# Performance work log

Measured on AMD Instinct MI355X. Metric: run time of the kernel, lower is better.

The kernel has to match this reference:

```python
import jax, jax.numpy as jnp
import numpy as np

B, C, N = 4, 256, 512
CQ = C // 4
SIGMA = 15.0
PICK = 0  # args.picked_point_num
FACTOR = 180.0 / (np.pi * SIGMA)
BN_EPS = 1e-5


def _angle_embed(angles, W, b):
    """SinusoidalPositionalEmbedding (interleaved sin/cos, detached) + Linear proj."""
    d = W.shape[0]
    div_term = jnp.exp(jnp.arange(0, d, 2, dtype=jnp.float32) * (-np.log(10000.0) / d))
    omegas = (angles * FACTOR)[..., None] * div_term  # (..., d/2)
    # torch cat([sin, cos], dim=2) on (-1, d/2, 1) then view -> interleaved [s0,c0,s1,c1,...]
    emb = jnp.stack([jnp.sin(omegas), jnp.cos(omegas)], axis=-1).reshape(*angles.shape, d)
    emb = jax.lax.stop_gradient(emb)  # .detach() in torch
    return emb @ W.T + b


def setup_inputs() -> dict:
    key = jax.random.key(0)
    ks = jax.random.split(key, 16)
    s = 0.05
    return {
        "x": jax.random.normal(ks[0], (B, C, N), jnp.float32),
        "pca": jax.random.normal(ks[1], (B, C, N), jnp.float32),
        "angle_lrf": jax.random.uniform(ks[2], (B, N, N), jnp.float32, 0.0, np.pi),
        "angle_pca": jax.random.uniform(ks[3], (B, N), jnp.float32, 0.0, np.pi),
        "Wkp": jax.random.normal(ks[4], (CQ, C), jnp.float32) * s,
        "Wk": jax.random.normal(ks[5], (CQ, C), jnp.float32) * s,
        "Wv": jax.random.normal(ks[6], (C, C), jnp.float32) * s,
        "Wvp": jax.random.normal(ks[7], (C, C), jnp.float32) * s,
        "emb1_W": jax.random.normal(ks[8], (CQ, CQ), jnp.float32) * s,
        "emb1_b": jnp.zeros((CQ,), jnp.float32),
        "emb2_W": jax.random.normal(ks[9], (CQ, CQ), jnp.float32) * s,
        "emb2_b": jnp.zeros((CQ,), jnp.float32),
        "lin_W": jax.random.normal(ks[10], (C, C), jnp.float32) * s,
        "lin_b": jnp.zeros((C,), jnp.float32),
        "bn_gamma": jnp.ones((C,), jnp.float32),
        "bn_beta": jnp.zeros((C,), jnp.float32),
    }


def reference(x, pca, angle_lrf, angle_pca, Wkp, Wk, Wv, Wvp,
              emb1_W, emb1_b, emb2_W, emb2_b, lin_W, lin_b, bn_gamma, bn_beta):
    # q uses the k_conv_pca weight (weight tying in __init__)
    x_q = jnp.einsum('oc,bcn->bno', Wkp, x)            # (B,N,CQ)
    k_lrf = jnp.einsum('oc,bcn->bon', Wk, x)           # (B,CQ,N)
    k_pca = jnp.einsum('oc,bcn->bon', Wkp, pca)        # (B,CQ,N)
    energy_lrf = jnp.einsum('bno,bom->bnm', x_q, k_lrf)
    energy_pca = jnp.einsum('bno,bom->bnm', x_q, k_pca)
    e1 = _angle_embed(angle_lrf, emb1_W, emb1_b)       # (B,N,N,CQ) relative-angle bias
    energy_lrf = energy_lrf + jnp.einsum('bnc,bnmc->bnm', x_q, e1)
    e2 = _angle_embed(angle_pca, emb2_W, emb2_b)       # (B,N,CQ)
    energy_pca = energy_pca + jnp.einsum('bnc,bmc->bnm', x_q, e2)
    energy = jax.nn.softmax(energy_lrf + energy_pca, axis=-1)
    # extra column renormalization
    energy = energy / (1e-12 + energy.sum(axis=1, keepdims=True))
    point_relation = energy[:, PICK:PICK + 1, :]       # (B,1,N)
    v_lrf = jnp.einsum('oc,bcn->bon', Wv, x)
    v_pca = jnp.einsum('oc,bcn->bon', Wvp, pca)
    x_lrf = jnp.einsum('bon,bnm->bom', v_lrf, energy)
    x_pca = jnp.einsum('bon,bnm->bom', v_pca, energy)
    x_r = 0.5 * x_lrf + 0.5 * x_pca
    z = jnp.einsum('oc,bcn->bon', lin_W, x - x_r) + lin_b[None, :, None]
    # BatchNorm1d (training-mode batch stats, biased var)
    mu = z.mean(axis=(0, 2), keepdims=True)
    var = z.var(axis=(0, 2), keepdims=True)
    y = bn_gamma[None, :, None] * (z - mu) * jax.lax.rsqrt(var + BN_EPS) + bn_beta[None, :, None]
    out = x + jax.nn.gelu(y, approximate=False)
    return out, point_relation
```

## Files before the change

### kernel.cpp

```cpp
#include <hip/hip_runtime.h>
#include <math.h>

#define FCT 3.81971863420548805845f
#define DIVK 0.28782313662425575f

using bf16x8 = __attribute__((ext_vector_type(8))) short;
using f32x4  = __attribute__((ext_vector_type(4))) float;

__device__ inline short f2bf(float f) {
    union { float f; unsigned u; } v; v.f = f;
    unsigned r = v.u + 0x7FFFu + ((v.u >> 16) & 1u);
    return (short)(r >> 16);
}
__device__ inline float bf2f(short s) {
    union { unsigned u; float f; } v;
    v.u = ((unsigned)(unsigned short)s) << 16;
    return v.f;
}
__device__ inline unsigned pk2(float lo, float hi) {
    return ((unsigned)(unsigned short)f2bf(hi) << 16) | (unsigned)(unsigned short)f2bf(lo);
}

__global__ __launch_bounds__(256) void k_prep(
    const float* __restrict__ Wkp, const float* __restrict__ Wk,
    const float* __restrict__ Wv, const float* __restrict__ Wvp,
    const float* __restrict__ linW, const float* __restrict__ e1W,
    const float* __restrict__ x, const float* __restrict__ pca,
    short* __restrict__ Wcatb, short* __restrict__ InTb)
{
    __shared__ float ts[64][65];
    const int bid = blockIdx.x;
    if (bid < 704) {
        const int r = bid;
        for (int k = threadIdx.x; k < 512; k += 256) {
            float v = 0.f;
            if (r < 64) { if (k < 256) v = Wkp[r*256 + k]; }
            else if (r < 128) { int o = r-64;  v = (k<256) ? Wk[o*256+k]  : Wkp[o*256 + k-256]; }
            else if (r < 384) { int o = r-128; v = (k<256) ? Wv[o*256+k]  : Wvp[o*256 + k-256]; }
            else if (r < 640) { int o = r-384; if (k<256) v = linW[o*256+k]; }
            else {
                int o = r-640;
                if (k < 256) {
                    float a = 0.f;
                    for (int j = 0; j < 64; ++j) a = fmaf(e1W[j*64 + o], Wkp[j*256 + k], a);
                    v = a;
                }
            }
            Wcatb[(size_t)r*512 + k] = f2bf(v);
        }
    } else {
        const int id = bid - 704;
        const int b  = id >> 6;
        const int kt = (id >> 3) & 7;
        const int nt = id & 7;
        const int k0 = kt*64, n0 = nt*64;
        const float* src = (k0 < 256) ? (x + ((size_t)b*256 + k0)*512)
                                      : (pca + ((size_t)b*256 + (k0-256))*512);
        #pragma unroll
        for (int i = 0; i < 16; ++i) {
            int idx = threadIdx.x + 256*i;
            int r = idx >> 6, c = idx & 63;
            ts[r][c] = src[(size_t)r*512 + n0 + c];
        }
        __syncthreads();
        short* dst = InTb + (size_t)b*512*512;
        #pragma unroll
        for (int i = 0; i < 16; ++i) {
            int idx = threadIdx.x + 256*i;
            int n = idx >> 6, k = idx & 63;
            dst[(size_t)(n0+n)*512 + k0 + k] = f2bf(ts[k][n]);
        }
    }
}

__global__ __launch_bounds__(256) void k_gemm1(
    const short* __restrict__ Wcatb, const short* __restrict__ InTb,
    short* __restrict__ xqb, float* __restrict__ Ktf, short* __restrict__ vsumb,
    float* __restrict__ linx, float* __restrict__ q1T)
{
    const int bid = blockIdx.x;
    const int b  = bid / 176;
    const int rt = (bid / 16) % 11;
    const int ct = bid % 16;
    const int r0 = rt*64, c0 = ct*32;
    const int w = threadIdx.x >> 6, lane = threadIdx.x & 63;
    const int lr = lane & 15, lg = lane >> 4;

    const short* ap  = Wcatb + (size_t)(r0 + w*16 + lr)*512 + 8*lg;
    const short* bp0 = InTb + (size_t)b*512*512 + (size_t)(c0 + lr)*512 + 8*lg;
    const short* bp1 = bp0 + 16*512;

    f32x4 acc0 = {0.f,0.f,0.f,0.f}, acc1 = {0.f,0.f,0.f,0.f};
    #pragma unroll 4
    for (int kk = 0; kk < 512; kk += 32) {
        bf16x8 a  = *(const bf16x8*)(ap  + kk);
        bf16x8 b0 = *(const bf16x8*)(bp0 + kk);
        bf16x8 b1 = *(const bf16x8*)(bp1 + kk);
        acc0 = __builtin_amdgcn_mfma_f32_16x16x32_bf16(a, b0, acc0, 0, 0, 0);
        acc1 = __builtin_amdgcn_mfma_f32_16x16x32_bf16(a, b1, acc1, 0, 0, 0);
    }
    const int rowb = r0 + w*16 + lg*4;
    const int col0 = c0 + lr;
    if (r0 == 0) {
        #pragma unroll
        for (int j = 0; j < 4; ++j) {
            xqb[((size_t)b*512 + col0)*64 + rowb + j]      = f2bf(acc0[j]);
            xqb[((size_t)b*512 + col0 + 16)*64 + rowb + j] = f2bf(acc1[j]);
        }
    } else if (r0 == 64) {
        #pragma unroll
        for (int j = 0; j < 4; ++j) {
            Ktf[((size_t)b*64 + rowb-64 + j)*512 + col0]      = acc0[j];
            Ktf[((size_t)b*64 + rowb-64 + j)*512 + col0 + 16] = acc1[j];
        }
    } else if (r0 < 384) {
        #pragma unroll
        for (int j = 0; j < 4; ++j) {
            vsumb[((size_t)b*256 + rowb-128 + j)*512 + col0]      = f2bf(acc0[j]);
            vsumb[((size_t)b*256 + rowb-128 + j)*512 + col0 + 16] = f2bf(acc1[j]);
        }
    } else if (r0 < 640) {
        #pragma unroll
        for (int j = 0; j < 4; ++j) {
            linx[((size_t)b*256 + rowb-384 + j)*512 + col0]      = acc0[j];
            linx[((size_t)b*256 + rowb-384 + j)*512 + col0 + 16] = acc1[j];
        }
    } else {
        #pragma unroll
        for (int j = 0; j < 4; ++j) {
            q1T[((size_t)b*512 + col0)*64 + rowb-640 + j]      = acc0[j];
            q1T[((size_t)b*512 + col0 + 16)*64 + rowb-640 + j] = acc1[j];
        }
    }
}

__global__ __launch_bounds__(256) void k_e2t(
    const float* __restrict__ angle_pca, const float* __restrict__ e2W,
    const float* __restrict__ Ktf, short* __restrict__ KtT)
{
    const int b  = blockIdx.x >> 3;
    const int m0 = (blockIdx.x & 7) * 64;
    __shared__ float emb_s[64][65];
    __shared__ float e2w_s[64][65];
    const int t = threadIdx.x;
    #pragma unroll
    for (int i = 0; i < 16; ++i) {
        int idx = t + 256*i;
        e2w_s[idx >> 6][idx & 63] = e2W[idx];
    }
    {
        const int m = t >> 2, q = t & 3;
        const float a = angle_pca[b*512 + m0 + m] * FCT;
        #pragma unroll
        for (int i = q*8; i < q*8+8; ++i) {
            float arg = a * __expf(-(float)i * DIVK);
            emb_s[m][2*i]   = __sinf(arg);
            emb_s[m][2*i+1] = __cosf(arg);
        }
    }
    __syncthreads();
    const int o = t & 63, wid = t >> 6;
    for (int mi = wid; mi < 64; mi += 4) {
        float acc = Ktf[((size_t)b*64 + o)*512 + m0 + mi];
        #pragma unroll 8
        for (int k = 0; k < 64; ++k) acc = fmaf(e2w_s[o][k], emb_s[mi][k], acc);
        KtT[((size_t)b*512 + m0 + mi)*64 + o] = f2bf(acc);
    }
}

__global__ __launch_bounds__(256) void k_qk(
    const short* __restrict__ xqb, const short* __restrict__ KtT,
    float* __restrict__ S)
{
    const int bid = blockIdx.x;
    const int b  = bid / 128;
    const int rt = (bid / 16) % 8;
    const int ct = bid % 16;
    const int r0 = rt*64, c0 = ct*32;
    const int w = threadIdx.x >> 6, lane = threadIdx.x & 63;
    const int lr = lane & 15, lg = lane >> 4;
    const short* ap  = xqb + ((size_t)b*512 + r0 + w*16 + lr)*64 + 8*lg;
    const short* bp0 = KtT + ((size_t)b*512 + c0 + lr)*64 + 8*lg;
    const short* bp1 = bp0 + 16*64;
    f32x4 acc0 = {0.f,0.f,0.f,0.f}, acc1 = {0.f,0.f,0.f,0.f};
    #pragma unroll
    for (int kk = 0; kk < 64; kk += 32) {
        bf16x8 a  = *(const bf16x8*)(ap  + kk);
        bf16x8 b0 = *(const bf16x8*)(bp0 + kk);
        bf16x8 b1 = *(const bf16x8*)(bp1 + kk);
        acc0 = __builtin_amdgcn_mfma_f32_16x16x32_bf16(a, b0, acc0, 0, 0, 0);
        acc1 = __builtin_amdgcn_mfma_f32_16x16x32_bf16(a, b1, acc1, 0, 0, 0);
    }
    const int rowb = r0 + w*16 + lg*4;
    const int col0 = c0 + lr;
    float* Sb = S + (size_t)b*512*512;
    #pragma unroll
    for (int j = 0; j < 4; ++j) {
        Sb[(size_t)(rowb+j)*512 + col0]      = acc0[j];
        Sb[(size_t)(rowb+j)*512 + col0 + 16] = acc1[j];
    }
}

__global__ __launch_bounds__(256) void k_energy2(
    const float* __restrict__ S, const float* __restrict__ q1T,
    const float* __restrict__ angle_lrf, short* __restrict__ ETb)
{
    const int b  = blockIdx.x >> 7;
    const int n0 = (blockIdx.x & 127) * 4;
    __shared__ float qs[4][64];
    __shared__ float divs[32];
    __shared__ float4 red[256];
    const int t = threadIdx.x;
    if (t < 64) {
        #pragma unroll
        for (int i = 0; i < 4; ++i) qs[i][t] = q1T[((size_t)b*512 + n0 + i)*64 + t];
    } else if (t < 96) {
        divs[t-64] = __expf(-(float)(t-64) * DIVK);
    }
    __syncthreads();
    float acc[4][2], av[4][2];
    #pragma unroll
    for (int i = 0; i < 4; ++i) {
        const float2 sv = *(const float2*)&S[((size_t)b*512 + n0 + i)*512 + 2*t];
        const float2 an = *(const float2*)&angle_lrf[((size_t)b*512 + n0 + i)*512 + 2*t];
        acc[i][0] = sv.x; acc[i][1] = sv.y;
        av[i][0] = an.x * FCT; av[i][1] = an.y * FCT;
    }
    for (int j = 0; j < 32; ++j) {
        const float d = divs[j];
        const float w0 = qs[0][2*j], w1 = qs[0][2*j+1];
        const float u0 = qs[1][2*j], u1 = qs[1][2*j+1];
        const float v0 = qs[2][2*j], v1 = qs[2][2*j+1];
        const float y0 = qs[3][2*j], y1 = qs[3][2*j+1];
        #pragma unroll
        for (int m = 0; m < 2; ++m) {
            float a0 = av[0][m]*d, a1 = av[1][m]*d, a2 = av[2][m]*d, a3 = av[3][m]*d;
            acc[0][m] = fmaf(w0, __sinf(a0), fmaf(w1, __cosf(a0), acc[0][m]));
            acc[1][m] = fmaf(u0, __sinf(a1), fmaf(u1, __cosf(a1), acc[1][m]));
            acc[2][m] = fmaf(v0, __sinf(a2), fmaf(v1, __cosf(a2), acc[2][m]));
            acc[3][m] = fmaf(y0, __sinf(a3), fmaf(y1, __cosf(a3), acc[3][m]));
        }
    }
    float4 v;
    v.x = fmaxf(acc[0][0], acc[0][1]); v.y = fmaxf(acc[1][0], acc[1][1]);
    v.z = fmaxf(acc[2][0], acc[2][1]); v.w = fmaxf(acc[3][0], acc[3][1]);
    red[t] = v; __syncthreads();
    for (int s = 128; s > 0; s >>= 1) {
        if (t < s) {
            float4 o = red[t+s], m2 = red[t];
            m2.x = fmaxf(m2.x,o.x); m2.y = fmaxf(m2.y,o.y);
            m2.z = fmaxf(m2.z,o.z); m2.w = fmaxf(m2.w,o.w);
            red[t] = m2;
        }
        __syncthreads();
    }
    const float4 mx = red[0]; __syncthreads();
    float p[4][2];
    p[0][0] = __expf(acc[0][0]-mx.x); p[0][1] = __expf(acc[0][1]-mx.x);
    p[1][0] = __expf(acc[1][0]-mx.y); p[1][1] = __expf(acc[1][1]-mx.y);
    p[2][0] = __expf(acc[2][0]-mx.z); p[2][1] = __expf(acc[2][1]-mx.z);
    p[3][0] = __expf(acc[3][0]-mx.w); p[3][1] = __expf(acc[3][1]-mx.w);
    v.x = p[0][0]+p[0][1]; v.y = p[1][0]+p[1][1];
    v.z = p[2][0]+p[2][1]; v.w = p[3][0]+p[3][1];
    red[t] = v; __syncthreads();
    for (int s = 128; s > 0; s >>= 1) {
        if (t < s) {
            float4 o = red[t+s];
            red[t].x += o.x; red[t].y += o.y; red[t].z += o.z; red[t].w += o.w;
        }
        __syncthreads();
    }
    const float4 tot = red[0];
    const float i0 = 1.f/tot.x, i1 = 1.f/tot.y, i2 = 1.f/tot.z, i3 = 1.f/tot.w;
    short* Eb = ETb + (size_t)b*512*512;
    #pragma unroll
    for (int m = 0; m < 2; ++m) {
        uint2 u;
        u.x = pk2(p[0][m]*i0, p[1][m]*i1);
        u.y = pk2(p[2][m]*i2, p[3][m]*i3);
        *(uint2*)(Eb + (size_t)(2*t + m)*512 + n0) = u;
    }
}

__global__ __launch_bounds__(256) void k_colsum(
    const short* __restrict__ ETb, float* __restrict__ rc, float* __restrict__ out)
{
    const int row  = blockIdx.x*4 + (threadIdx.x >> 6);
    const int lane = threadIdx.x & 63;
    const uint4 u4 = *(const uint4*)(ETb + (size_t)row*512 + lane*8);
    float s = 0.f;
    unsigned uu[4] = {u4.x, u4.y, u4.z, u4.w};
    #pragma unroll
    for (int i = 0; i < 4; ++i) {
        union { unsigned u; float f; } lo, hi;
        lo.u = uu[i] << 16; hi.u = uu[i] & 0xFFFF0000u;
        s += lo.f + hi.f;
    }
    #pragma unroll
    for (int off = 32; off > 0; off >>= 1) s += __shfl_xor(s, off, 64);
    if (lane == 0) {
        const float r = 1.f / (1e-12f + s);
        rc[row] = r;
        out[(size_t)4*256*512 + row] = bf2f((short)(u4.x & 0xFFFFu)) * r;
    }
}

__global__ __launch_bounds__(256) void k_xr2(
    const short* __restrict__ vsumb, const short* __restrict__ ETb,
    const float* __restrict__ rc, short* __restrict__ xrT)
{
    const int bid = blockIdx.x;
    const int b  = bid / 64;
    const int rt = (bid / 16) % 4;
    const int ct = bid % 16;
    const int r0 = rt*64, c0 = ct*32;
    const int w = threadIdx.x >> 6, lane = threadIdx.x & 63;
    const int lr = lane & 15, lg = lane >> 4;
    const short* ap  = vsumb + (size_t)b*256*512 + (size_t)(r0 + w*16 + lr)*512 + 8*lg;
    const short* bp0 = ETb + (size_t)b*512*512 + (size_t)(c0 + lr)*512 + 8*lg;
    const short* bp1 = bp0 + 16*512;
    f32x4 acc0 = {0.f,0.f,0.f,0.f}, acc1 = {0.f,0.f,0.f,0.f};
    #pragma unroll 4
    for (int kk = 0; kk < 512; kk += 32) {
        bf16x8 a  = *(const bf16x8*)(ap  + kk);
        bf16x8 b0 = *(const bf16x8*)(bp0 + kk);
        bf16x8 b1 = *(const bf16x8*)(bp1 + kk);
        acc0 = __builtin_amdgcn_mfma_f32_16x16x32_bf16(a, b0, acc0, 0, 0, 0);
        acc1 = __builtin_amdgcn_mfma_f32_16x16x32_bf16(a, b1, acc1, 0, 0, 0);
    }
    const int rowb = r0 + w*16 + lg*4;
    const int m0 = c0 + lr, m1 = m0 + 16;
    const float s0 = 0.5f * rc[b*512 + m0];
    const float s1 = 0.5f * rc[b*512 + m1];
    short* xb = xrT + (size_t)b*512*256;
    uint2 u;
    u.x = pk2(acc0[0]*s0, acc0[1]*s0);
    u.y = pk2(acc0[2]*s0, acc0[3]*s0);
    *(uint2*)(xb + (size_t)m0*256 + rowb) = u;
    u.x = pk2(acc1[0]*s1, acc1[1]*s1);
    u.y = pk2(acc1[2]*s1, acc1[3]*s1);
    *(uint2*)(xb + (size_t)m1*256 + rowb) = u;
}

__global__ __launch_bounds__(256) void k_z2(
    const short* __restrict__ Wcatb, const short* __restrict__ xrT,
    const float* __restrict__ linx, const float* __restrict__ lin_b,
    float* __restrict__ z)
{
    const int bid = blockIdx.x;
    const int b  = bid / 64;
    const int rt = (bid / 16) % 4;
    const int ct = bid % 16;
    const int r0 = rt*64, c0 = ct*32;
    const int w = threadIdx.x >> 6, lane = threadIdx.x & 63;
    const int lr = lane & 15, lg = lane >> 4;
    const short* ap  = Wcatb + (size_t)(384 + r0 + w*16 + lr)*512 + 8*lg;
    const short* bp0 = xrT + (size_t)b*512*256 + (size_t)(c0 + lr)*256 + 8*lg;
    const short* bp1 = bp0 + 16*256;
    f32x4 acc0 = {0.f,0.f,0.f,0.f}, acc1 = {0.f,0.f,0.f,0.f};
    #pragma unroll
    for (int kk = 0; kk < 256; kk += 32) {
        bf16x8 a  = *(const bf16x8*)(ap  + kk);
        bf16x8 b0 = *(const bf16x8*)(bp0 + kk);
        bf16x8 b1 = *(const bf16x8*)(bp1 + kk);
        acc0 = __builtin_amdgcn_mfma_f32_16x16x32_bf16(a, b0, acc0, 0, 0, 0);
        acc1 = __builtin_amdgcn_mfma_f32_16x16x32_bf16(a, b1, acc1, 0, 0, 0);
    }
    const int rowb = r0 + w*16 + lg*4;
    const int col0 = c0 + lr;
    const float* Lb = linx + (size_t)b*256*512;
    float* zb = z + (size_t)b*256*512;
    #pragma unroll
    for (int j = 0; j < 4; ++j) {
        float lb = lin_b[rowb+j];
        zb[(size_t)(rowb+j)*512 + col0]      = Lb[(size_t)(rowb+j)*512 + col0]      - acc0[j] + lb;
        zb[(size_t)(rowb+j)*512 + col0 + 16] = Lb[(size_t)(rowb+j)*512 + col0 + 16] - acc1[j] + lb;
    }
}

__global__ __launch_bounds__(256) void k_stats(
    const float* __restrict__ z, float* __restrict__ stat)
{
    const int c = blockIdx.x;
    const int t = threadIdx.x;
    float s = 0.f, s2 = 0.f;
    for (int i = t; i < 2048; i += 256) {
        int b = i >> 9, n = i & 511;
        float v = z[((size_t)b*256 + c)*512 + n];
        s += v; s2 = fmaf(v, v, s2);
    }
    __shared__ float r1[256], r2[256];
    r1[t] = s; r2[t] = s2;
    __syncthreads();
    for (int st = 128; st > 0; st >>= 1) {
        if (t < st) { r1[t] += r1[t+st]; r2[t] += r2[t+st]; }
        __syncthreads();
    }
    if (t == 0) { stat[c] = r1[0]; stat[256 + c] = r2[0]; }
}

__global__ __launch_bounds__(256) void k_final(
    const float* __restrict__ x, const float* __restrict__ z,
    const float* __restrict__ stat, const float* __restrict__ gamma,
    const float* __restrict__ beta, float* __restrict__ out)
{
    const int gid = blockIdx.x*256 + threadIdx.x;
    const int base = gid * 4;
    const int c = (base >> 9) & 255;
    const float mu  = stat[c] * (1.f/2048.f);
    const float var = stat[256 + c] * (1.f/2048.f) - mu*mu;
    const float gsc = gamma[c] * rsqrtf(var + 1e-5f);
    const float bt  = beta[c];
    const float4 zv = *(const float4*)&z[base];
    const float4 xv = *(const float4*)&x[base];
    float4 ov;
    {
        float y = (zv.x - mu)*gsc + bt;
        ov.x = xv.x + 0.5f*y*(1.f + erff(y*0.70710678118654752f));
        y = (zv.y - mu)*gsc + bt;
        ov.y = xv.y + 0.5f*y*(1.f + erff(y*0.70710678118654752f));
        y = (zv.z - mu)*gsc + bt;
        ov.z = xv.z + 0.5f*y*(1.f + erff(y*0.70710678118654752f));
        y = (zv.w - mu)*gsc + bt;
        ov.w = xv.w + 0.5f*y*(1.f + erff(y*0.70710678118654752f));
    }
    *(float4*)&out[base] = ov;
}

extern "C" void kernel_launch(void* const* d_in, const int* in_sizes, int n_in,
                              void* d_out, int out_size, void* d_ws, size_t ws_size,
                              hipStream_t stream)
{
    const float* x         = (const float*)d_in[0];
    const float* pca       = (const float*)d_in[1];
    const float* angle_lrf = (const float*)d_in[2];
    const float* angle_pca = (const float*)d_in[3];
    const float* Wkp       = (const float*)d_in[4];
    const float* Wk        = (const float*)d_in[5];
    const float* Wv        = (const float*)d_in[6];
    const float* Wvp       = (const float*)d_in[7];
    const float* e1W       = (const float*)d_in[8];
    const float* e2W       = (const float*)d_in[10];
    const float* linW      = (const float*)d_in[12];
    const float* linb      = (const float*)d_in[13];
    const float* gamma     = (const float*)d_in[14];
    const float* beta      = (const float*)d_in[15];

    char* w = (char*)d_ws;
    short* Wcatb = (short*)(w + 0);
    short* InTb  = (short*)(w + 720896);
    short* vsumb = (short*)(w + 2818048);
    short* KtT   = (short*)(w + 3866624);
    short* ETb   = (short*)(w + 4128768);
    float* rc    = (float*)(w + 6225920);
    short* xrT   = (short*)(w + 6234112);
    float* stat  = (float*)(w + 7282688);
    float* S     = (float*)(w + 7284736);
    float* Ktf   = (float*)(w + 7284736);
    float* z     = (float*)(w + 7284736);
    short* xqb   = (short*)(w + 11479040);
    float* q1T   = (float*)(w + 11741184);
    float* linx  = (float*)(w + 12789760);
    float* out   = (float*)d_out;

    k_prep   <<<960, 256, 0, stream>>>(Wkp, Wk, Wv, Wvp, linW, e1W, x, pca, Wcatb, InTb);
    k_gemm1  <<<704, 256, 0, stream>>>(Wcatb, InTb, xqb, Ktf, vsumb, linx, q1T);
    k_e2t    <<<32,  256, 0, stream>>>(angle_pca, e2W, Ktf, KtT);
    k_qk     <<<512, 256, 0, stream>>>(xqb, KtT, S);
    k_energy2<<<512, 256, 0, stream>>>(S, q1T, angle_lrf, ETb);
    k_colsum <<<512, 256, 0, stream>>>(ETb, rc, out);
    k_xr2    <<<256, 256, 0, stream>>>(vsumb, ETb, rc, xrT);
    k_z2     <<<256, 256, 0, stream>>>(Wcatb, xrT, linx, linb, z);
    k_stats  <<<256, 256, 0, stream>>>(z, stat);
    k_final  <<<512, 256, 0, stream>>>(x, z, stat, gamma, beta, out);
}
```

Baseline: 88.00 us.

## Fuse colsum and BN stats into producers, use native revolution sin/cos

Removes the separate column-sum and BatchNorm-statistics kernels. Their work moves into k_energy2 and the z GEMM as atomicAdd accumulations, with buffers zeroed in k_prep. The energy and embedding kernels call hardware v_sin/v_cos on arguments pre-scaled to revolutions, avoiding range reduction. The block max/sum reductions become wave shuffles. The e2 projection is restructured with a transposed weight and register accumulation, and k_prep processes 4 rows per block. Atomics add nondeterministic summation order and contention on colsum, and there is accuracy risk from the raw sin/cos instructions.

```diff
diff --git a/kernel.cpp b/kernel.cpp
--- a/kernel.cpp
+++ b/kernel.cpp
@@ -1,7 +1,7 @@
 #include <hip/hip_runtime.h>
 #include <math.h>
 
-#define FCT 3.81971863420548805845f
+#define FCT_REV 0.6079271018540267f
 #define DIVK 0.28782313662425575f
 
 using bf16x8 = __attribute__((ext_vector_type(8))) short;
@@ -20,36 +20,57 @@
 __device__ inline unsigned pk2(float lo, float hi) {
     return ((unsigned)(unsigned short)f2bf(hi) << 16) | (unsigned)(unsigned short)f2bf(lo);
 }
+__device__ inline float sinrev(float x) {
+    float r; asm("v_sin_f32 %0, %1" : "=v"(r) : "v"(x)); return r;
+}
+__device__ inline float cosrev(float x) {
+    float r; asm("v_cos_f32 %0, %1" : "=v"(r) : "v"(x)); return r;
+}
 
 __global__ __launch_bounds__(256) void k_prep(
     const float* __restrict__ Wkp, const float* __restrict__ Wk,
     const float* __restrict__ Wv, const float* __restrict__ Wvp,
     const float* __restrict__ linW, const float* __restrict__ e1W,
+    const float* __restrict__ e2W,
     const float* __restrict__ x, const float* __restrict__ pca,
-    short* __restrict__ Wcatb, short* __restrict__ InTb)
+    short* __restrict__ Wcatb, short* __restrict__ InTb,
+    float* __restrict__ e2Wt, float* __restrict__ stat, float* __restrict__ colsum)
 {
     __shared__ float ts[64][65];
     const int bid = blockIdx.x;
-    if (bid < 704) {
-        const int r = bid;
-        for (int k = threadIdx.x; k < 512; k += 256) {
-            float v = 0.f;
-            if (r < 64) { if (k < 256) v = Wkp[r*256 + k]; }
-            else if (r < 128) { int o = r-64;  v = (k<256) ? Wk[o*256+k]  : Wkp[o*256 + k-256]; }
-            else if (r < 384) { int o = r-128; v = (k<256) ? Wv[o*256+k]  : Wvp[o*256 + k-256]; }
-            else if (r < 640) { int o = r-384; if (k<256) v = linW[o*256+k]; }
-            else {
-                int o = r-640;
-                if (k < 256) {
-                    float a = 0.f;
-                    for (int j = 0; j < 64; ++j) a = fmaf(e1W[j*64 + o], Wkp[j*256 + k], a);
-                    v = a;
+    const int t = threadIdx.x;
+    if (bid < 176) {
+        if (bid == 0) {
+            for (int i = t; i < 2048; i += 256) colsum[i] = 0.f;
+            for (int i = t; i < 512; i += 256) stat[i] = 0.f;
+        } else if (bid == 1) {
+            for (int i = t; i < 4096; i += 256) {
+                int k = i >> 6, o = i & 63;
+                e2Wt[k*64 + o] = e2W[o*64 + k];
+            }
+        }
+        #pragma unroll
+        for (int rr = 0; rr < 4; ++rr) {
+            const int r = bid*4 + rr;
+            for (int k = t; k < 512; k += 256) {
+                float v = 0.f;
+                if (r < 64) { if (k < 256) v = Wkp[r*256 + k]; }
+                else if (r < 128) { int o = r-64;  v = (k<256) ? Wk[o*256+k]  : Wkp[o*256 + k-256]; }
+                else if (r < 384) { int o = r-128; v = (k<256) ? Wv[o*256+k]  : Wvp[o*256 + k-256]; }
+                else if (r < 640) { int o = r-384; if (k<256) v = linW[o*256+k]; }
+                else {
+                    int o = r-640;
+                    if (k < 256) {
+                        float a = 0.f;
+                        for (int j = 0; j < 64; ++j) a = fmaf(e1W[j*64 + o], Wkp[j*256 + k], a);
+                        v = a;
+                    }
                 }
+                Wcatb[(size_t)r*512 + k] = f2bf(v);
             }
-            Wcatb[(size_t)r*512 + k] = f2bf(v);
         }
     } else {
-        const int id = bid - 704;
+        const int id = bid - 176;
         const int b  = id >> 6;
         const int kt = (id >> 3) & 7;
         const int nt = id & 7;
@@ -58,7 +79,7 @@
                                       : (pca + ((size_t)b*256 + (k0-256))*512);
         #pragma unroll
         for (int i = 0; i < 16; ++i) {
-            int idx = threadIdx.x + 256*i;
+            int idx = t + 256*i;
             int r = idx >> 6, c = idx & 63;
             ts[r][c] = src[(size_t)r*512 + n0 + c];
         }
@@ -66,7 +87,7 @@
         short* dst = InTb + (size_t)b*512*512;
         #pragma unroll
         for (int i = 0; i < 16; ++i) {
-            int idx = threadIdx.x + 256*i;
+            int idx = t + 256*i;
             int n = idx >> 6, k = idx & 63;
             dst[(size_t)(n0+n)*512 + k0 + k] = f2bf(ts[k][n]);
         }
@@ -75,7 +96,7 @@
 
 __global__ __launch_bounds__(256) void k_gemm1(
     const short* __restrict__ Wcatb, const short* __restrict__ InTb,
-    short* __restrict__ xqb, float* __restrict__ Ktf, short* __restrict__ vsumb,
+    short* __restrict__ xqb, float* __restrict__ KtTf, short* __restrict__ vsumb,
     float* __restrict__ linx, float* __restrict__ q1T)
 {
     const int bid = blockIdx.x;
@@ -108,11 +129,10 @@
             xqb[((size_t)b*512 + col0 + 16)*64 + rowb + j] = f2bf(acc1[j]);
         }
     } else if (r0 == 64) {
-        #pragma unroll
-        for (int j = 0; j < 4; ++j) {
-            Ktf[((size_t)b*64 + rowb-64 + j)*512 + col0]      = acc0[j];
-            Ktf[((size_t)b*64 + rowb-64 + j)*512 + col0 + 16] = acc1[j];
-        }
+        float4 v0 = {acc0[0], acc0[1], acc0[2], acc0[3]};
+        float4 v1 = {acc1[0], acc1[1], acc1[2], acc1[3]};
+        *(float4*)&KtTf[((size_t)b*512 + col0)*64 + rowb - 64]      = v0;
+        *(float4*)&KtTf[((size_t)b*512 + col0 + 16)*64 + rowb - 64] = v1;
     } else if (r0 < 384) {
         #pragma unroll
         for (int j = 0; j < 4; ++j) {
@@ -134,38 +154,44 @@
     }
 }
 
-__global__ __launch_bounds__(256) void k_e2t(
-    const float* __restrict__ angle_pca, const float* __restrict__ e2W,
-    const float* __restrict__ Ktf, short* __restrict__ KtT)
+__global__ __launch_bounds__(256) void k_e2t2(
+    const float* __restrict__ angle_pca, const float* __restrict__ e2Wt,
+    const float* __restrict__ KtTf, short* __restrict__ KtT)
 {
     const int b  = blockIdx.x >> 3;
     const int m0 = (blockIdx.x & 7) * 64;
-    __shared__ float emb_s[64][65];
-    __shared__ float e2w_s[64][65];
+    __shared__ float embs[64][65];
     const int t = threadIdx.x;
-    #pragma unroll
-    for (int i = 0; i < 16; ++i) {
-        int idx = t + 256*i;
-        e2w_s[idx >> 6][idx & 63] = e2W[idx];
-    }
     {
         const int m = t >> 2, q = t & 3;
-        const float a = angle_pca[b*512 + m0 + m] * FCT;
-        #pragma unroll
-        for (int i = q*8; i < q*8+8; ++i) {
-            float arg = a * __expf(-(float)i * DIVK);
-            emb_s[m][2*i]   = __sinf(arg);
-            emb_s[m][2*i+1] = __cosf(arg);
+        const float arev = angle_pca[b*512 + m0 + m] * FCT_REV;
+        #pragma unroll
+        for (int j = q*8; j < q*8+8; ++j) {
+            float arg = arev * __expf(-(float)j * DIVK);
+            embs[m][2*j]   = sinrev(arg);
+            embs[m][2*j+1] = cosrev(arg);
         }
     }
     __syncthreads();
-    const int o = t & 63, wid = t >> 6;
-    for (int mi = wid; mi < 64; mi += 4) {
-        float acc = Ktf[((size_t)b*64 + o)*512 + m0 + mi];
-        #pragma unroll 8
-        for (int k = 0; k < 64; ++k) acc = fmaf(e2w_s[o][k], emb_s[mi][k], acc);
-        KtT[((size_t)b*512 + m0 + mi)*64 + o] = f2bf(acc);
-    }
+    const int lane = t & 63;
+    const int wv = __builtin_amdgcn_readfirstlane(t >> 6);
+    const int m = lane;
+    float acc[16];
+    const float* kt = KtTf + ((size_t)b*512 + m0 + m)*64 + 16*wv;
+    #pragma unroll
+    for (int oi = 0; oi < 16; ++oi) acc[oi] = kt[oi];
+    const float* wbase = e2Wt + 16*wv;
+    #pragma unroll 4
+    for (int k = 0; k < 64; ++k) {
+        const float em = embs[m][k];
+        const float* wr = wbase + (size_t)k*64;
+        #pragma unroll
+        for (int oi = 0; oi < 16; ++oi) acc[oi] = fmaf(wr[oi], em, acc[oi]);
+    }
+    short* dst = KtT + ((size_t)b*512 + m0 + m)*64 + 16*wv;
+    #pragma unroll
+    for (int oi = 0; oi < 16; oi += 2)
+        *(unsigned*)(dst + oi) = pk2(acc[oi], acc[oi+1]);
 }
 
 __global__ __launch_bounds__(256) void k_qk(
@@ -201,15 +227,16 @@
     }
 }
 
-__global__ __launch_bounds__(256) void k_energy2(
+__global__ __launch_bounds__(256, 2) void k_energy2(
     const float* __restrict__ S, const float* __restrict__ q1T,
-    const float* __restrict__ angle_lrf, short* __restrict__ ETb)
+    const float* __restrict__ angle_lrf, short* __restrict__ ETb,
+    float* __restrict__ colsum)
 {
     const int b  = blockIdx.x >> 7;
     const int n0 = (blockIdx.x & 127) * 4;
     __shared__ float qs[4][64];
     __shared__ float divs[32];
-    __shared__ float4 red[256];
+    __shared__ float4 xw[4];
     const int t = threadIdx.x;
     if (t < 64) {
         #pragma unroll
@@ -224,90 +251,79 @@
         const float2 sv = *(const float2*)&S[((size_t)b*512 + n0 + i)*512 + 2*t];
         const float2 an = *(const float2*)&angle_lrf[((size_t)b*512 + n0 + i)*512 + 2*t];
         acc[i][0] = sv.x; acc[i][1] = sv.y;
-        av[i][0] = an.x * FCT; av[i][1] = an.y * FCT;
-    }
+        av[i][0] = an.x * FCT_REV; av[i][1] = an.y * FCT_REV;
+    }
+    #pragma unroll 2
     for (int j = 0; j < 32; ++j) {
         const float d = divs[j];
-        const float w0 = qs[0][2*j], w1 = qs[0][2*j+1];
-        const float u0 = qs[1][2*j], u1 = qs[1][2*j+1];
-        const float v0 = qs[2][2*j], v1 = qs[2][2*j+1];
-        const float y0 = qs[3][2*j], y1 = qs[3][2*j+1];
-        #pragma unroll
-        for (int m = 0; m < 2; ++m) {
-            float a0 = av[0][m]*d, a1 = av[1][m]*d, a2 = av[2][m]*d, a3 = av[3][m]*d;
-            acc[0][m] = fmaf(w0, __sinf(a0), fmaf(w1, __cosf(a0), acc[0][m]));
-            acc[1][m] = fmaf(u0, __sinf(a1), fmaf(u1, __cosf(a1), acc[1][m]));
-            acc[2][m] = fmaf(v0, __sinf(a2), fmaf(v1, __cosf(a2), acc[2][m]));
-            acc[3][m] = fmaf(y0, __sinf(a3), fmaf(y1, __cosf(a3), acc[3][m]));
-        }
-    }
-    float4 v;
-    v.x = fmaxf(acc[0][0], acc[0][1]); v.y = fmaxf(acc[1][0], acc[1][1]);
-    v.z = fmaxf(acc[2][0], acc[2][1]); v.w = fmaxf(acc[3][0], acc[3][1]);
-    red[t] = v; __syncthreads();
-    for (int s = 128; s > 0; s >>= 1) {
-        if (t < s) {
-            float4 o = red[t+s], m2 = red[t];
-            m2.x = fmaxf(m2.x,o.x); m2.y = fmaxf(m2.y,o.y);
-            m2.z = fmaxf(m2.z,o.z); m2.w = fmaxf(m2.w,o.w);
-            red[t] = m2;
-        }
-        __syncthreads();
-    }
-    const float4 mx = red[0]; __syncthreads();
+        #pragma unroll
+        for (int i = 0; i < 4; ++i) {
+            const float q0 = qs[i][2*j], q1 = qs[i][2*j+1];
+            #pragma unroll
+            for (int m = 0; m < 2; ++m) {
+                const float arg = av[i][m] * d;
+                acc[i][m] = fmaf(q0, sinrev(arg), fmaf(q1, cosrev(arg), acc[i][m]));
+            }
+        }
+    }
+    float v0 = fmaxf(acc[0][0], acc[0][1]), v1 = fmaxf(acc[1][0], acc[1][1]);
+    float v2 = fmaxf(acc[2][0], acc[2][1]), v3 = fmaxf(acc[3][0], acc[3][1]);
+    #pragma unroll
+    for (int off = 1; off < 64; off <<= 1) {
+        v0 = fmaxf(v0, __shfl_xor(v0, off));
+        v1 = fmaxf(v1, __shfl_xor(v1, off));
+        v2 = fmaxf(v2, __shfl_xor(v2, off));
+        v3 = fmaxf(v3, __shfl_xor(v3, off));
+    }
+    const int wid = t >> 6, lane = t & 63;
+    if (lane == 0) { float4 f = {v0,v1,v2,v3}; xw[wid] = f; }
+    __syncthreads();
+    {
+        const float4 a0 = xw[0], a1 = xw[1], a2 = xw[2], a3 = xw[3];
+        v0 = fmaxf(fmaxf(a0.x,a1.x), fmaxf(a2.x,a3.x));
+        v1 = fmaxf(fmaxf(a0.y,a1.y), fmaxf(a2.y,a3.y));
+        v2 = fmaxf(fmaxf(a0.z,a1.z), fmaxf(a2.z,a3.z));
+        v3 = fmaxf(fmaxf(a0.w,a1.w), fmaxf(a2.w,a3.w));
+    }
     float p[4][2];
-    p[0][0] = __expf(acc[0][0]-mx.x); p[0][1] = __expf(acc[0][1]-mx.x);
-    p[1][0] = __expf(acc[1][0]-mx.y); p[1][1] = __expf(acc[1][1]-mx.y);
-    p[2][0] = __expf(acc[2][0]-mx.z); p[2][1] = __expf(acc[2][1]-mx.z);
-    p[3][0] = __expf(acc[3][0]-mx.w); p[3][1] = __expf(acc[3][1]-mx.w);
-    v.x = p[0][0]+p[0][1]; v.y = p[1][0]+p[1][1];
-    v.z = p[2][0]+p[2][1]; v.w = p[3][0]+p[3][1];
-    red[t] = v; __syncthreads();
-    for (int s = 128; s > 0; s >>= 1) {
-        if (t < s) {
-            float4 o = red[t+s];
-            red[t].x += o.x; red[t].y += o.y; red[t].z += o.z; red[t].w += o.w;
-        }
-        __syncthreads();
-    }
-    const float4 tot = red[0];
-    const float i0 = 1.f/tot.x, i1 = 1.f/tot.y, i2 = 1.f/tot.z, i3 = 1.f/tot.w;
+    p[0][0] = __expf(acc[0][0]-v0); p[0][1] = __expf(acc[0][1]-v0);
+    p[1][0] = __expf(acc[1][0]-v1); p[1][1] = __expf(acc[1][1]-v1);
+    p[2][0] = __expf(acc[2][0]-v2); p[2][1] = __expf(acc[2][1]-v2);
+    p[3][0] = __expf(acc[3][0]-v3); p[3][1] = __expf(acc[3][1]-v3);
+    float s0 = p[0][0]+p[0][1], s1 = p[1][0]+p[1][1];
+    float s2 = p[2][0]+p[2][1], s3 = p[3][0]+p[3][1];
+    #pragma unroll
+    for (int off = 1; off < 64; off <<= 1) {
+        s0 += __shfl_xor(s0, off); s1 += __shfl_xor(s1, off);
+        s2 += __shfl_xor(s2, off); s3 += __shfl_xor(s3, off);
+    }
+    __syncthreads();
+    if (lane == 0) { float4 f = {s0,s1,s2,s3}; xw[wid] = f; }
+    __syncthreads();
+    {
+        const float4 a0 = xw[0], a1 = xw[1], a2 = xw[2], a3 = xw[3];
+        s0 = (a0.x+a1.x) + (a2.x+a3.x);
+        s1 = (a0.y+a1.y) + (a2.y+a3.y);
+        s2 = (a0.z+a1.z) + (a2.z+a3.z);
+        s3 = (a0.w+a1.w) + (a2.w+a3.w);
+    }
+    const float i0 = 1.f/s0, i1 = 1.f/s1, i2 = 1.f/s2, i3 = 1.f/s3;
     short* Eb = ETb + (size_t)b*512*512;
     #pragma unroll
     for (int m = 0; m < 2; ++m) {
+        const float e0 = p[0][m]*i0, e1 = p[1][m]*i1, e2 = p[2][m]*i2, e3 = p[3][m]*i3;
         uint2 u;
-        u.x = pk2(p[0][m]*i0, p[1][m]*i1);
-        u.y = pk2(p[2][m]*i2, p[3][m]*i3);
+        u.x = pk2(e0, e1);
+        u.y = pk2(e2, e3);
         *(uint2*)(Eb + (size_t)(2*t + m)*512 + n0) = u;
-    }
-}
-
-__global__ __launch_bounds__(256) void k_colsum(
-    const short* __restrict__ ETb, float* __restrict__ rc, float* __restrict__ out)
-{
-    const int row  = blockIdx.x*4 + (threadIdx.x >> 6);
-    const int lane = threadIdx.x & 63;
-    const uint4 u4 = *(const uint4*)(ETb + (size_t)row*512 + lane*8);
-    float s = 0.f;
-    unsigned uu[4] = {u4.x, u4.y, u4.z, u4.w};
-    #pragma unroll
-    for (int i = 0; i < 4; ++i) {
-        union { unsigned u; float f; } lo, hi;
-        lo.u = uu[i] << 16; hi.u = uu[i] & 0xFFFF0000u;
-        s += lo.f + hi.f;
-    }
-    #pragma unroll
-    for (int off = 32; off > 0; off >>= 1) s += __shfl_xor(s, off, 64);
-    if (lane == 0) {
-        const float r = 1.f / (1e-12f + s);
-        rc[row] = r;
-        out[(size_t)4*256*512 + row] = bf2f((short)(u4.x & 0xFFFFu)) * r;
+        atomicAdd(&colsum[b*512 + 2*t + m], (e0 + e1) + (e2 + e3));
     }
 }
 
 __global__ __launch_bounds__(256) void k_xr2(
     const short* __restrict__ vsumb, const short* __restrict__ ETb,
-    const float* __restrict__ rc, short* __restrict__ xrT)
+    const float* __restrict__ colsum, short* __restrict__ xrT,
+    float* __restrict__ out)
 {
     const int bid = blockIdx.x;
     const int b  = bid / 64;
@@ -330,8 +346,9 @@
     }
     const int rowb = r0 + w*16 + lg*4;
     const int m0 = c0 + lr, m1 = m0 + 16;
-    const float s0 = 0.5f * rc[b*512 + m0];
-    const float s1 = 0.5f * rc[b*512 + m1];
+    const float rc0 = 1.f / (1e-12f + colsum[b*512 + m0]);
+    const float rc1 = 1.f / (1e-12f + colsum[b*512 + m1]);
+    const float s0 = 0.5f * rc0, s1 = 0.5f * rc1;
     short* xb = xrT + (size_t)b*512*256;
     uint2 u;
     u.x = pk2(acc0[0]*s0, acc0[1]*s0);
@@ -340,12 +357,16 @@
     u.x = pk2(acc1[0]*s1, acc1[1]*s1);
     u.y = pk2(acc1[2]*s1, acc1[3]*s1);
     *(uint2*)(xb + (size_t)m1*256 + rowb) = u;
-}
-
-__global__ __launch_bounds__(256) void k_z2(
+    if (w == 0 && lg == 0) {
+        out[(size_t)4*256*512 + b*512 + m0] = bf2f(ETb[((size_t)b*512 + m0)*512]) * rc0;
+        out[(size_t)4*256*512 + b*512 + m1] = bf2f(ETb[((size_t)b*512 + m1)*512]) * rc1;
+    }
+}
+
+__global__ __launch_bounds__(256) void k_z2st(
     const short* __restrict__ Wcatb, const short* __restrict__ xrT,
     const float* __restrict__ linx, const float* __restrict__ lin_b,
-    float* __restrict__ z)
+    float* __restrict__ z, float* __restrict__ stat)
 {
     const int bid = blockIdx.x;
     const int b  = bid / 64;
@@ -372,31 +393,23 @@
     float* zb = z + (size_t)b*256*512;
     #pragma unroll
     for (int j = 0; j < 4; ++j) {
-        float lb = lin_b[rowb+j];
-        zb[(size_t)(rowb+j)*512 + col0]      = Lb[(size_t)(rowb+j)*512 + col0]      - acc0[j] + lb;
-        zb[(size_t)(rowb+j)*512 + col0 + 16] = Lb[(size_t)(rowb+j)*512 + col0 + 16] - acc1[j] + lb;
-    }
-}
-
-__global__ __launch_bounds__(256) void k_stats(
-    const float* __restrict__ z, float* __restrict__ stat)
-{
-    const int c = blockIdx.x;
-    const int t = threadIdx.x;
-    float s = 0.f, s2 = 0.f;
-    for (int i = t; i < 2048; i += 256) {
-        int b = i >> 9, n = i & 511;
-        float v = z[((size_t)b*256 + c)*512 + n];
-        s += v; s2 = fmaf(v, v, s2);
-    }
-    __shared__ float r1[256], r2[256];
-    r1[t] = s; r2[t] = s2;
-    __syncthreads();
-    for (int st = 128; st > 0; st >>= 1) {
-        if (t < st) { r1[t] += r1[t+st]; r2[t] += r2[t+st]; }
-        __syncthreads();
-    }
-    if (t == 0) { stat[c] = r1[0]; stat[256 + c] = r2[0]; }
+        const float lb = lin_b[rowb+j];
+        const float z0 = Lb[(size_t)(rowb+j)*512 + col0]      - acc0[j] + lb;
+        const float z1 = Lb[(size_t)(rowb+j)*512 + col0 + 16] - acc1[j] + lb;
+        zb[(size_t)(rowb+j)*512 + col0]      = z0;
+        zb[(size_t)(rowb+j)*512 + col0 + 16] = z1;
+        float s  = z0 + z1;
+        float s2 = z0*z0 + z1*z1;
+        #pragma unroll
+        for (int off = 1; off < 16; off <<= 1) {
+            s  += __shfl_xor(s,  off);
+            s2 += __shfl_xor(s2, off);
+        }
+        if (lr == 0) {
+            atomicAdd(&stat[rowb+j], s);
+            atomicAdd(&stat[256 + rowb+j], s2);
+        }
+    }
 }
 
 __global__ __launch_bounds__(256) void k_final(
@@ -447,30 +460,30 @@
     const float* beta      = (const float*)d_in[15];
 
     char* w = (char*)d_ws;
-    short* Wcatb = (short*)(w + 0);
-    short* InTb  = (short*)(w + 720896);
-    short* vsumb = (short*)(w + 2818048);
-    short* KtT   = (short*)(w + 3866624);
-    short* ETb   = (short*)(w + 4128768);
-    float* rc    = (float*)(w + 6225920);
-    short* xrT   = (short*)(w + 6234112);
-    float* stat  = (float*)(w + 7282688);
-    float* S     = (float*)(w + 7284736);
-    float* Ktf   = (float*)(w + 7284736);
-    float* z     = (float*)(w + 7284736);
-    short* xqb   = (short*)(w + 11479040);
-    float* q1T   = (float*)(w + 11741184);
-    float* linx  = (float*)(w + 12789760);
-    float* out   = (float*)d_out;
-
-    k_prep   <<<960, 256, 0, stream>>>(Wkp, Wk, Wv, Wvp, linW, e1W, x, pca, Wcatb, InTb);
-    k_gemm1  <<<704, 256, 0, stream>>>(Wcatb, InTb, xqb, Ktf, vsumb, linx, q1T);
-    k_e2t    <<<32,  256, 0, stream>>>(angle_pca, e2W, Ktf, KtT);
+    short* Wcatb  = (short*)(w + 0);
+    short* InTb   = (short*)(w + 720896);
+    short* vsumb  = (short*)(w + 2818048);
+    short* KtT    = (short*)(w + 3866624);
+    short* ETb    = (short*)(w + 4128768);
+    short* xrT    = (short*)(w + 6225920);
+    float* stat   = (float*)(w + 7274496);
+    float* colsum = (float*)(w + 7276544);
+    float* S      = (float*)(w + 7284736);
+    float* e2Wt   = (float*)(w + 7284736);
+    float* z      = (float*)(w + 7284736);
+    float* KtTf   = (float*)(w + 11479040);
+    short* xqb    = (short*)(w + 12003328);
+    float* q1T    = (float*)(w + 12265472);
+    float* linx   = (float*)(w + 12789760);
+    float* out    = (float*)d_out;
+
+    k_prep   <<<432, 256, 0, stream>>>(Wkp, Wk, Wv, Wvp, linW, e1W, e2W, x, pca,
+                                       Wcatb, InTb, e2Wt, stat, colsum);
+    k_gemm1  <<<704, 256, 0, stream>>>(Wcatb, InTb, xqb, KtTf, vsumb, linx, q1T);
+    k_e2t2   <<<32,  256, 0, stream>>>(angle_pca, e2Wt, KtTf, KtT);
     k_qk     <<<512, 256, 0, stream>>>(xqb, KtT, S);
-    k_energy2<<<512, 256, 0, stream>>>(S, q1T, angle_lrf, ETb);
-    k_colsum <<<512, 256, 0, stream>>>(ETb, rc, out);
-    k_xr2    <<<256, 256, 0, stream>>>(vsumb, ETb, rc, xrT);
-    k_z2     <<<256, 256, 0, stream>>>(Wcatb, xrT, linx, linb, z);
-    k_stats  <<<256, 256, 0, stream>>>(z, stat);
+    k_energy2<<<512, 256, 0, stream>>>(S, q1T, angle_lrf, ETb, colsum);
+    k_xr2    <<<256, 256, 0, stream>>>(vsumb, ETb, colsum, xrT, out);
+    k_z2st   <<<256, 256, 0, stream>>>(Wcatb, xrT, linx, linb, z, stat);
     k_final  <<<512, 256, 0, stream>>>(x, z, stat, gamma, beta, out);
 }
```

After: 89.16 us. No clear change (+1.3%).
